# Kernel optimization log

Measured on AMD Instinct MI355X. Metric: run time of the kernel, lower is better.

## Reference

```python
import jax, jax.numpy as jnp
import numpy as np


def _bilinear_warp(img, flo):
    """Flow-shifted bilinear grid sample (channels_last), matching tf_warp.

    img: [B, H, W, C] float
    flo: [B, H, W, 2] float, (dx, dy) pixel offsets
    """
    B, H, W, C = img.shape
    gy, gx = jnp.meshgrid(jnp.arange(H, dtype=flo.dtype),
                          jnp.arange(W, dtype=flo.dtype), indexing='ij')
    # sampling coordinates = base grid + flow
    x = gx[None] + flo[..., 0]   # [B,H,W]
    y = gy[None] + flo[..., 1]   # [B,H,W]

    x0f = jnp.floor(x)
    y0f = jnp.floor(y)
    wx = x - x0f                 # fractional weights in [0,1)
    wy = y - y0f

    x0 = jnp.clip(x0f.astype(jnp.int32), 0, W - 1)
    x1 = jnp.clip(x0f.astype(jnp.int32) + 1, 0, W - 1)
    y0 = jnp.clip(y0f.astype(jnp.int32), 0, H - 1)
    y1 = jnp.clip(y0f.astype(jnp.int32) + 1, 0, H - 1)

    b = jnp.arange(B)[:, None, None]  # batch index for gather
    Ia = img[b, y0, x0]  # top-left
    Ib = img[b, y1, x0]  # bottom-left
    Ic = img[b, y0, x1]  # top-right
    Id = img[b, y1, x1]  # bottom-right

    wa = ((1.0 - wx) * (1.0 - wy))[..., None]
    wb = ((1.0 - wx) * wy)[..., None]
    wc = (wx * (1.0 - wy))[..., None]
    wd = (wx * wy)[..., None]
    return wa * Ia + wb * Ib + wc * Ic + wd * Id


def setup_inputs() -> dict:
    key = jax.random.key(0)
    k1, k2 = jax.random.split(key)
    img = jax.random.normal(k1, (8, 384, 512, 64), dtype=jnp.float32)
    # flow magnitudes ~ tens of pixels, typical for optical flow
    flo = jax.random.normal(k2, (8, 384, 512, 2), dtype=jnp.float32) * 10.0
    return {"img": img, "flo": flo}


def reference(img, flo):
    return _bilinear_warp(img, flo)
```

## Files before the change

kernel.cpp:

```cpp
#include <hip/hip_runtime.h>


constexpr int B = 8, H = 384, W = 512, C = 64;
constexpr long long NPIX = (long long)B * H * W;

__global__ __launch_bounds__(256) void warp_bilinear_kernel(
    const float* __restrict__ img,
    const float* __restrict__ flo,
    float* __restrict__ out)
{
    long long tid = (long long)blockIdx.x * blockDim.x + threadIdx.x;
    long long p = tid >> 4;
    int cq = (int)(tid & 15) << 2;
    if (p >= NPIX) return;

    int x_i = (int)(p % W);
    long long yb = p / W;
    int y_i = (int)(yb % H);
    int b   = (int)(yb / H);

    float2 f = *reinterpret_cast<const float2*>(flo + p * 2);
    float x = (float)x_i + f.x;
    float y = (float)y_i + f.y;

    float x0f = floorf(x);
    float y0f = floorf(y);
    float wx = x - x0f;
    float wy = y - y0f;

    int x0 = min(max((int)x0f, 0), W - 1);
    int x1 = min(max((int)x0f + 1, 0), W - 1);
    int y0 = min(max((int)y0f, 0), H - 1);
    int y1 = min(max((int)y0f + 1, 0), H - 1);

    const float* base = img + (long long)b * H * W * C + cq;
    const float4 Ia = *reinterpret_cast<const float4*>(base + ((long long)y0 * W + x0) * C);
    const float4 Ib = *reinterpret_cast<const float4*>(base + ((long long)y1 * W + x0) * C);
    const float4 Ic = *reinterpret_cast<const float4*>(base + ((long long)y0 * W + x1) * C);
    const float4 Id = *reinterpret_cast<const float4*>(base + ((long long)y1 * W + x1) * C);

    float wa = (1.0f - wx) * (1.0f - wy);
    float wb = (1.0f - wx) * wy;
    float wc = wx * (1.0f - wy);
    float wd = wx * wy;

    float4 r;
    r.x = wa * Ia.x + wb * Ib.x + wc * Ic.x + wd * Id.x;
    r.y = wa * Ia.y + wb * Ib.y + wc * Ic.y + wd * Id.y;
    r.z = wa * Ia.z + wb * Ib.z + wc * Ic.z + wd * Id.z;
    r.w = wa * Ia.w + wb * Ib.w + wc * Ic.w + wd * Id.w;

    *reinterpret_cast<float4*>(out + p * C + cq) = r;
}

extern "C" void kernel_launch(void* const* d_in, const int* in_sizes, int n_in,
                              void* d_out, int out_size, void* d_ws, size_t ws_size,
                              hipStream_t stream) {
    const float* img = (const float*)d_in[0];
    const float* flo = (const float*)d_in[1];
    float* out = (float*)d_out;

    long long total_threads = NPIX * 16;
    int block = 256;
    long long grid = (total_threads + block - 1) / block;
    warp_bilinear_kernel<<<(int)grid, block, 0, stream>>>(img, flo, out);
}
```

Baseline: 198.2 us.

## Use 3D grid, 8 threads per pixel with two float4s, nontemporal stores

Replaces the flat 1D indexing, which needed 64-bit div/mod, with a 3D grid (x tiles of 32 pixels, y, batch). Each thread now handles 8 channels as two float4 halves instead of one float4, so each pixel's flow is loaded by 8 threads instead of 16. Flow loads and output stores use nontemporal hints to keep streaming data from polluting the cache that serves the image gathers. The cost is fewer threads per pixel and more registers per thread.

```diff
diff --git a/kernel.cpp b/kernel.cpp
--- a/kernel.cpp
+++ b/kernel.cpp
@@ -2,24 +2,24 @@
 
 
 constexpr int B = 8, H = 384, W = 512, C = 64;
-constexpr long long NPIX = (long long)B * H * W;
+
+typedef float f4 __attribute__((ext_vector_type(4)));
+typedef float f2 __attribute__((ext_vector_type(2)));
 
 __global__ __launch_bounds__(256) void warp_bilinear_kernel(
     const float* __restrict__ img,
     const float* __restrict__ flo,
     float* __restrict__ out)
 {
-    long long tid = (long long)blockIdx.x * blockDim.x + threadIdx.x;
-    long long p = tid >> 4;
-    int cq = (int)(tid & 15) << 2;
-    if (p >= NPIX) return;
+    int lane = threadIdx.x & 7;
+    int pix  = threadIdx.x >> 3;
+    int x_i = blockIdx.x * 32 + pix;
+    int y_i = blockIdx.y;
+    int b   = blockIdx.z;
 
-    int x_i = (int)(p % W);
-    long long yb = p / W;
-    int y_i = (int)(yb % H);
-    int b   = (int)(yb / H);
+    long long p = ((long long)b * H + y_i) * (long long)W + x_i;
 
-    float2 f = *reinterpret_cast<const float2*>(flo + p * 2);
+    f2 f = __builtin_nontemporal_load(reinterpret_cast<const f2*>(flo + p * 2));
     float x = (float)x_i + f.x;
     float y = (float)y_i + f.y;
 
@@ -33,24 +33,32 @@
     int y0 = min(max((int)y0f, 0), H - 1);
     int y1 = min(max((int)y0f + 1, 0), H - 1);
 
-    const float* base = img + (long long)b * H * W * C + cq;
-    const float4 Ia = *reinterpret_cast<const float4*>(base + ((long long)y0 * W + x0) * C);
-    const float4 Ib = *reinterpret_cast<const float4*>(base + ((long long)y1 * W + x0) * C);
-    const float4 Ic = *reinterpret_cast<const float4*>(base + ((long long)y0 * W + x1) * C);
-    const float4 Id = *reinterpret_cast<const float4*>(base + ((long long)y1 * W + x1) * C);
+    const float* base = img + (long long)b * H * W * C + (lane << 2);
+    const float* pa = base + ((long long)y0 * W + x0) * C;
+    const float* pb = base + ((long long)y1 * W + x0) * C;
+    const float* pc = base + ((long long)y0 * W + x1) * C;
+    const float* pd = base + ((long long)y1 * W + x1) * C;
+
+    f4 Ia0 = *reinterpret_cast<const f4*>(pa);
+    f4 Ia1 = *reinterpret_cast<const f4*>(pa + 32);
+    f4 Ib0 = *reinterpret_cast<const f4*>(pb);
+    f4 Ib1 = *reinterpret_cast<const f4*>(pb + 32);
+    f4 Ic0 = *reinterpret_cast<const f4*>(pc);
+    f4 Ic1 = *reinterpret_cast<const f4*>(pc + 32);
+    f4 Id0 = *reinterpret_cast<const f4*>(pd);
+    f4 Id1 = *reinterpret_cast<const f4*>(pd + 32);
 
     float wa = (1.0f - wx) * (1.0f - wy);
     float wb = (1.0f - wx) * wy;
     float wc = wx * (1.0f - wy);
     float wd = wx * wy;
 
-    float4 r;
-    r.x = wa * Ia.x + wb * Ib.x + wc * Ic.x + wd * Id.x;
-    r.y = wa * Ia.y + wb * Ib.y + wc * Ic.y + wd * Id.y;
-    r.z = wa * Ia.z + wb * Ib.z + wc * Ic.z + wd * Id.z;
-    r.w = wa * Ia.w + wb * Ib.w + wc * Ic.w + wd * Id.w;
+    f4 r0 = wa * Ia0 + wb * Ib0 + wc * Ic0 + wd * Id0;
+    f4 r1 = wa * Ia1 + wb * Ib1 + wc * Ic1 + wd * Id1;
 
-    *reinterpret_cast<float4*>(out + p * C + cq) = r;
+    float* op = out + p * C + (lane << 2);
+    __builtin_nontemporal_store(r0, reinterpret_cast<f4*>(op));
+    __builtin_nontemporal_store(r1, reinterpret_cast<f4*>(op + 32));
 }
 
 extern "C" void kernel_launch(void* const* d_in, const int* in_sizes, int n_in,
@@ -60,8 +68,7 @@
     const float* flo = (const float*)d_in[1];
     float* out = (float*)d_out;
 
-    long long total_threads = NPIX * 16;
-    int block = 256;
-    long long grid = (total_threads + block - 1) / block;
-    warp_bilinear_kernel<<<(int)grid, block, 0, stream>>>(img, flo, out);
+    dim3 grid(W / 32, H, B);
+    dim3 block(256);
+    warp_bilinear_kernel<<<grid, block, 0, stream>>>(img, flo, out);
 }
```

After: 182.2 us. -8.1%, faster.
